# Kernel optimization log

Hardware: AMD Instinct MI355X
Metric: run time of the kernel (lower is better)

Reference implementation:

```python
import jax, jax.numpy as jnp
import numpy as np


def _conv_valid(x, w):
    # x: [B, Cin, H, W], w: [Cout, Cin, K, K], stride 1, no padding
    return jax.lax.conv_general_dilated(
        x, w, window_strides=(1, 1), padding='VALID',
        dimension_numbers=('NCHW', 'OIHW', 'NCHW'))


def _buggy_maxpool(x, k=2):
    # Faithful to the source MaxPool: window of size kxk slides with STRIDE 1,
    # but only the first H//k x W//k positions are kept (top-left region).
    nh = x.shape[2] // k
    nw = x.shape[3] // k
    m = jax.lax.reduce_window(
        x, -jnp.inf, jax.lax.max,
        window_dimensions=(1, 1, k, k),
        window_strides=(1, 1, 1, 1),
        padding='VALID')  # [B, C, H-k+1, W-k+1]
    return m[:, :, :nh, :nw]


def setup_inputs() -> dict:
    key = jax.random.key(0)
    ks = jax.random.split(key, 9)
    B = 8192
    x = jax.random.normal(ks[0], (B, 3, 32, 32), dtype=jnp.float32)
    s = 0.1
    conv1_w = jax.random.normal(ks[1], (6, 3, 5, 5), dtype=jnp.float32) * s
    conv2_w = jax.random.normal(ks[2], (16, 6, 5, 5), dtype=jnp.float32) * s
    fc1_w = jax.random.normal(ks[3], (120, 400), dtype=jnp.float32) * s
    fc1_b = jax.random.normal(ks[4], (120,), dtype=jnp.float32) * s
    fc2_w = jax.random.normal(ks[5], (84, 120), dtype=jnp.float32) * s
    fc2_b = jax.random.normal(ks[6], (84,), dtype=jnp.float32) * s
    fc3_w = jax.random.normal(ks[7], (10, 84), dtype=jnp.float32) * s
    fc3_b = jax.random.normal(ks[8], (10,), dtype=jnp.float32) * s
    return {
        'x': x,
        'conv1_w': conv1_w, 'conv2_w': conv2_w,
        'fc1_w': fc1_w, 'fc1_b': fc1_b,
        'fc2_w': fc2_w, 'fc2_b': fc2_b,
        'fc3_w': fc3_w, 'fc3_b': fc3_b,
    }


def reference(x, conv1_w, conv2_w, fc1_w, fc1_b, fc2_w, fc2_b, fc3_w, fc3_b):
    h = _buggy_maxpool(jax.nn.relu(_conv_valid(x, conv1_w)))   # [B,6,14,14]
    h = _buggy_maxpool(jax.nn.relu(_conv_valid(h, conv2_w)))   # [B,16,5,5]
    h = h.reshape(-1, 16 * 5 * 5)                              # [B,400]
    h = jax.nn.relu(h @ fc1_w.T + fc1_b)                       # [B,120]
    h = jax.nn.relu(h @ fc2_w.T + fc2_b)                       # [B,84]
    return h @ fc3_w.T + fc3_b                                 # [B,10]
```

## Files before the change

kernel.cpp:

```cpp
#include <hip/hip_runtime.h>


typedef float v2f __attribute__((ext_vector_type(2)));
__device__ __forceinline__ v2f mk2(float a, float b) { v2f t; t.x = a; t.y = b; return t; }
__device__ __forceinline__ v2f shfl2(v2f v, int src) {
    v2f r; r.x = __shfl(v.x, src, 64); r.y = __shfl(v.y, src, 64); return r;
}

constexpr int THREADS = 256;
constexpr int IPB = 8;

constexpr int W1P_OFF = 0;
constexpr int W2P_OFF = 452;
constexpr int IMG_BASE = 2852;
constexpr int XS_OFF = 0;
constexpr int P1_OFF = 0;
constexpr int P2_OFF = 0;
constexpr int F1_OFF = 0;
constexpr int F2_OFF = 128;
constexpr int IMG_STRIDE = 720;
constexpr int LDS_FLOATS = IMG_BASE + IPB * IMG_STRIDE;

__device__ __forceinline__ void wave_sync() {
    asm volatile("s_waitcnt lgkmcnt(0)" ::: "memory");
}

extern "C" __global__ __launch_bounds__(THREADS, 4)
void lenet_fused(const float* __restrict__ x,
                 const float* __restrict__ w1,
                 const float* __restrict__ w2,
                 const float* __restrict__ fc1w, const float* __restrict__ fc1b,
                 const float* __restrict__ fc2w, const float* __restrict__ fc2b,
                 const float* __restrict__ fc3w, const float* __restrict__ fc3b,
                 float* __restrict__ out)
{
    __shared__ __align__(16) float lds[LDS_FLOATS];
    const int tid  = threadIdx.x;
    const int lane = tid & 63;
    const int wv   = tid >> 6;
    const int img0 = blockIdx.x * IPB;
    const v2f zero2 = mk2(0.f, 0.f);

    for (int i = tid; i < 450; i += THREADS) {
        int ocp = i / 150, rem = i - ocp * 150, k = rem >> 1, h = rem & 1;
        lds[W1P_OFF + i] = w1[(2 * ocp + h) * 75 + k];
    }
    for (int i = tid; i < 2400; i += THREADS) {
        int ocp = i / 300, rem = i - ocp * 300, k = rem >> 1, h = rem & 1;
        lds[W2P_OFF + i] = w2[(2 * ocp + h) * 150 + k];
    }

    float* baseA = lds + IMG_BASE + (wv * 2) * IMG_STRIDE;
    float* baseB = baseA + IMG_STRIDE;
    {
        const float4* xgA = (const float4*)(x + (size_t)(img0 + wv * 2) * 3072);
        const float4* xgB = (const float4*)(x + (size_t)(img0 + wv * 2 + 1) * 3072);
        float4* dA = (float4*)(baseA + XS_OFF);
        float4* dB = (float4*)(baseB + XS_OFF);
        for (int i = lane; i < 180; i += 64) {
            int c = i / 60, rem = i - c * 60;
            int r = rem >> 2, c4 = rem & 3;
            int src = c * 256 + r * 8 + c4;
            dA[i] = xgA[src];
            dB[i] = xgB[src];
        }
    }
    __syncthreads();

    float* p1A = baseA + P1_OFF;
    float* p1B = baseB + P1_OFF;

    {
        const int l   = (lane < 33) ? lane : 32;
        const int ocp = l / 11;
        const int r   = l - ocp * 11;
        const float4* xsA = (const float4*)(baseA + XS_OFF);
        const float4* xsB = (const float4*)(baseB + XS_OFF);
        const v2f* w1p = (const v2f*)(lds + W1P_OFF);

        v2f accA[11], accB[11];
        #pragma unroll
        for (int c = 0; c < 11; ++c) { accA[c] = zero2; accB[c] = zero2; }

        #pragma unroll
        for (int i = 0; i < 15; ++i) {
            const int ci = i / 5, kr = i - ci * 5;
            const int b = ci * 60 + (r + kr) * 4;
            float4 A0 = xsA[b], A1 = xsA[b + 1], A2 = xsA[b + 2], A3 = xsA[b + 3];
            float4 B0 = xsB[b], B1 = xsB[b + 1], B2 = xsB[b + 2], B3 = xsB[b + 3];
            v2f W[5];
            #pragma unroll
            for (int kc = 0; kc < 5; ++kc) W[kc] = w1p[ocp * 75 + i * 5 + kc];
            float xa[16], xb[16];
            xa[0]=A0.x; xa[1]=A0.y; xa[2]=A0.z;  xa[3]=A0.w;
            xa[4]=A1.x; xa[5]=A1.y; xa[6]=A1.z;  xa[7]=A1.w;
            xa[8]=A2.x; xa[9]=A2.y; xa[10]=A2.z; xa[11]=A2.w;
            xa[12]=A3.x; xa[13]=A3.y; xa[14]=A3.z; xa[15]=A3.w;
            xb[0]=B0.x; xb[1]=B0.y; xb[2]=B0.z;  xb[3]=B0.w;
            xb[4]=B1.x; xb[5]=B1.y; xb[6]=B1.z;  xb[7]=B1.w;
            xb[8]=B2.x; xb[9]=B2.y; xb[10]=B2.z; xb[11]=B2.w;
            xb[12]=B3.x; xb[13]=B3.y; xb[14]=B3.z; xb[15]=B3.w;
            #pragma unroll
            for (int kc = 0; kc < 5; ++kc) {
                #pragma unroll
                for (int c = 0; c < 11; ++c) {
                    accA[c] = __builtin_elementwise_fma(
                        mk2(xa[c + kc], xa[c + kc]), W[kc], accA[c]);
                    accB[c] = __builtin_elementwise_fma(
                        mk2(xb[c + kc], xb[c + kc]), W[kc], accB[c]);
                }
            }
        }

        v2f pmA[10], pmB[10], mA[10], mB[10];
        #pragma unroll
        for (int c = 0; c < 10; ++c) {
            v2f aA0 = __builtin_elementwise_max(accA[c], zero2);
            v2f aA1 = __builtin_elementwise_max(accA[c + 1], zero2);
            pmA[c] = __builtin_elementwise_max(aA0, aA1);
            v2f aB0 = __builtin_elementwise_max(accB[c], zero2);
            v2f aB1 = __builtin_elementwise_max(accB[c + 1], zero2);
            pmB[c] = __builtin_elementwise_max(aB0, aB1);
        }
        #pragma unroll
        for (int c = 0; c < 10; ++c) {
            mA[c] = __builtin_elementwise_max(pmA[c], shfl2(pmA[c], lane + 1));
            mB[c] = __builtin_elementwise_max(pmB[c], shfl2(pmB[c], lane + 1));
        }
        wave_sync();
        if (r < 10) {
            const int oc0 = ocp * 2;
            float2* dA0 = (float2*)(p1A + oc0 * 120 + r * 12);
            float2* dA1 = (float2*)(p1A + (oc0 + 1) * 120 + r * 12);
            float2* dB0 = (float2*)(p1B + oc0 * 120 + r * 12);
            float2* dB1 = (float2*)(p1B + (oc0 + 1) * 120 + r * 12);
            #pragma unroll
            for (int j = 0; j < 5; ++j) {
                dA0[j] = make_float2(mA[2 * j].x, mA[2 * j + 1].x);
                dA1[j] = make_float2(mA[2 * j].y, mA[2 * j + 1].y);
                dB0[j] = make_float2(mB[2 * j].x, mB[2 * j + 1].x);
                dB1[j] = make_float2(mB[2 * j].y, mB[2 * j + 1].y);
            }
        }
    }
    wave_sync();

    float* p2A = baseA + P2_OFF;
    float* p2B = baseB + P2_OFF;
    {
        const int l   = (lane < 48) ? lane : 47;
        const int ocp = l / 6;
        const int r   = l - ocp * 6;
        const float4* pA4 = (const float4*)p1A;
        const float2* pA2 = (const float2*)p1A;
        const float4* pB4 = (const float4*)p1B;
        const float2* pB2 = (const float2*)p1B;
        const v2f* w2p = (const v2f*)(lds + W2P_OFF);

        v2f accA[6], accB[6];
        #pragma unroll
        for (int c = 0; c < 6; ++c) { accA[c] = zero2; accB[c] = zero2; }

        #pragma unroll
        for (int i = 0; i < 30; ++i) {
            const int ci = i / 5, kr = i - ci * 5;
            float4 A0 = pA4[ci * 30 + (r + kr) * 3 + 0];
            float4 A1 = pA4[ci * 30 + (r + kr) * 3 + 1];
            float2 A2 = pA2[ci * 60 + (r + kr) * 6 + 4];
            float4 B0 = pB4[ci * 30 + (r + kr) * 3 + 0];
            float4 B1 = pB4[ci * 30 + (r + kr) * 3 + 1];
            float2 B2 = pB2[ci * 60 + (r + kr) * 6 + 4];
            v2f W[5];
            #pragma unroll
            for (int kc = 0; kc < 5; ++kc) W[kc] = w2p[ocp * 150 + i * 5 + kc];
            float xa[10], xb[10];
            xa[0]=A0.x; xa[1]=A0.y; xa[2]=A0.z; xa[3]=A0.w;
            xa[4]=A1.x; xa[5]=A1.y; xa[6]=A1.z; xa[7]=A1.w;
            xa[8]=A2.x; xa[9]=A2.y;
            xb[0]=B0.x; xb[1]=B0.y; xb[2]=B0.z; xb[3]=B0.w;
            xb[4]=B1.x; xb[5]=B1.y; xb[6]=B1.z; xb[7]=B1.w;
            xb[8]=B2.x; xb[9]=B2.y;
            #pragma unroll
            for (int kc = 0; kc < 5; ++kc) {
                #pragma unroll
                for (int c = 0; c < 6; ++c) {
                    accA[c] = __builtin_elementwise_fma(
                        mk2(xa[c + kc], xa[c + kc]), W[kc], accA[c]);
                    accB[c] = __builtin_elementwise_fma(
                        mk2(xb[c + kc], xb[c + kc]), W[kc], accB[c]);
                }
            }
        }

        v2f pmA[5], pmB[5], mA[5], mB[5];
        #pragma unroll
        for (int c = 0; c < 5; ++c) {
            v2f aA0 = __builtin_elementwise_max(accA[c], zero2);
            v2f aA1 = __builtin_elementwise_max(accA[c + 1], zero2);
            pmA[c] = __builtin_elementwise_max(aA0, aA1);
            v2f aB0 = __builtin_elementwise_max(accB[c], zero2);
            v2f aB1 = __builtin_elementwise_max(accB[c + 1], zero2);
            pmB[c] = __builtin_elementwise_max(aB0, aB1);
        }
        #pragma unroll
        for (int c = 0; c < 5; ++c) {
            mA[c] = __builtin_elementwise_max(pmA[c], shfl2(pmA[c], lane + 1));
            mB[c] = __builtin_elementwise_max(pmB[c], shfl2(pmB[c], lane + 1));
        }
        wave_sync();
        if (r < 5) {
            const int oc0 = ocp * 2;
            #pragma unroll
            for (int c = 0; c < 5; ++c) {
                p2A[oc0 * 25 + r * 5 + c]       = mA[c].x;
                p2A[(oc0 + 1) * 25 + r * 5 + c] = mA[c].y;
                p2B[oc0 * 25 + r * 5 + c]       = mB[c].x;
                p2B[(oc0 + 1) * 25 + r * 5 + c] = mB[c].y;
            }
        }
    }
    __syncthreads();

    float* scr = lds;
    if (tid < 240) {
        const int row  = tid >> 1;
        const int half = tid & 1;
        const float4* wrow = (const float4*)(fc1w + row * 400) + half * 50;
        v2f acc[8];
        #pragma unroll
        for (int im = 0; im < 8; ++im) acc[im] = zero2;
        #pragma unroll 2
        for (int k = 0; k < 50; ++k) {
            float4 w4 = wrow[k];
            const v2f wxy = mk2(w4.x, w4.y), wzw = mk2(w4.z, w4.w);
            #pragma unroll
            for (int im = 0; im < 8; ++im) {
                const float4* ap = (const float4*)(lds + IMG_BASE + im * IMG_STRIDE + P2_OFF) + half * 50;
                float4 a = ap[k];
                acc[im] = __builtin_elementwise_fma(mk2(a.x, a.y), wxy, acc[im]);
                acc[im] = __builtin_elementwise_fma(mk2(a.z, a.w), wzw, acc[im]);
            }
        }
        #pragma unroll
        for (int im = 0; im < 8; ++im)
            scr[im * 240 + row * 2 + half] = acc[im].x + acc[im].y;
    }
    __syncthreads();

    if (tid < 120) {
        const float b = fc1b[tid];
        #pragma unroll
        for (int im = 0; im < 8; ++im) {
            float v = scr[im * 240 + tid * 2] + scr[im * 240 + tid * 2 + 1] + b;
            lds[IMG_BASE + im * IMG_STRIDE + F1_OFF + tid] = fmaxf(v, 0.f);
        }
    }
    __syncthreads();

    if (tid < 84) {
        const int row = tid;
        const float4* wrow = (const float4*)(fc2w + row * 120);
        const float bz = fc2b[row];
        v2f acc[8];
        #pragma unroll
        for (int im = 0; im < 8; ++im) acc[im] = zero2;
        #pragma unroll 2
        for (int k = 0; k < 30; ++k) {
            float4 w4 = wrow[k];
            const v2f wxy = mk2(w4.x, w4.y), wzw = mk2(w4.z, w4.w);
            #pragma unroll
            for (int im = 0; im < 8; ++im) {
                const float4* fp = (const float4*)(lds + IMG_BASE + im * IMG_STRIDE + F1_OFF);
                float4 a = fp[k];
                acc[im] = __builtin_elementwise_fma(mk2(a.x, a.y), wxy, acc[im]);
                acc[im] = __builtin_elementwise_fma(mk2(a.z, a.w), wzw, acc[im]);
            }
        }
        #pragma unroll
        for (int im = 0; im < 8; ++im)
            lds[IMG_BASE + im * IMG_STRIDE + F2_OFF + row] =
                fmaxf(acc[im].x + acc[im].y + bz, 0.f);
    }
    __syncthreads();

    if (tid < 80) {
        const int im  = tid / 10;
        const int row = tid - im * 10;
        const float4* wrow = (const float4*)(fc3w + row * 84);
        const float4* f2 = (const float4*)(lds + IMG_BASE + im * IMG_STRIDE + F2_OFF);
        v2f acc = zero2;
        #pragma unroll
        for (int k = 0; k < 21; ++k) {
            float4 w4 = wrow[k];
            float4 a = f2[k];
            acc = __builtin_elementwise_fma(mk2(a.x, a.y), mk2(w4.x, w4.y), acc);
            acc = __builtin_elementwise_fma(mk2(a.z, a.w), mk2(w4.z, w4.w), acc);
        }
        out[(size_t)(img0 + im) * 10 + row] = acc.x + acc.y + fc3b[row];
    }
}

extern "C" void kernel_launch(void* const* d_in, const int* in_sizes, int n_in,
                              void* d_out, int out_size, void* d_ws, size_t ws_size,
                              hipStream_t stream) {
    const float* x    = (const float*)d_in[0];
    const float* w1   = (const float*)d_in[1];
    const float* w2   = (const float*)d_in[2];
    const float* fc1w = (const float*)d_in[3];
    const float* fc1b = (const float*)d_in[4];
    const float* fc2w = (const float*)d_in[5];
    const float* fc2b = (const float*)d_in[6];
    const float* fc3w = (const float*)d_in[7];
    const float* fc3b = (const float*)d_in[8];
    float* out = (float*)d_out;

    const int B = in_sizes[0] / 3072;
    const int grid = B / IPB;
    lenet_fused<<<grid, THREADS, 0, stream>>>(x, w1, w2, fc1w, fc1b,
                                              fc2w, fc2b, fc3w, fc3b, out);
}
```

Measured before the change: 214.4 us.

## Use one wave per image with 512 threads and padded input layout

Doubles the block to 512 threads so each of the 8 waves handles one image through both conv stages instead of two. The input tile is stored with a padded row stride (5 float4 per row, 75 per channel) and the per-image LDS stride grows to 900 floats. FC1 and FC2 are split across twice as many threads, each covering 4 images. This lowers per-thread register pressure and raises the number of resident waves, at the cost of a larger LDS footprint per block and more work repeated per wave (weight loads, index math).

```diff
diff --git a/kernel.cpp b/kernel.cpp
--- a/kernel.cpp
+++ b/kernel.cpp
@@ -7,7 +7,7 @@
     v2f r; r.x = __shfl(v.x, src, 64); r.y = __shfl(v.y, src, 64); return r;
 }
 
-constexpr int THREADS = 256;
+constexpr int THREADS = 512;
 constexpr int IPB = 8;
 
 constexpr int W1P_OFF = 0;
@@ -18,14 +18,14 @@
 constexpr int P2_OFF = 0;
 constexpr int F1_OFF = 0;
 constexpr int F2_OFF = 128;
-constexpr int IMG_STRIDE = 720;
+constexpr int IMG_STRIDE = 900;
 constexpr int LDS_FLOATS = IMG_BASE + IPB * IMG_STRIDE;
 
 __device__ __forceinline__ void wave_sync() {
     asm volatile("s_waitcnt lgkmcnt(0)" ::: "memory");
 }
 
-extern "C" __global__ __launch_bounds__(THREADS, 4)
+extern "C" __global__ __launch_bounds__(THREADS, 8)
 void lenet_fused(const float* __restrict__ x,
                  const float* __restrict__ w1,
                  const float* __restrict__ w2,
@@ -50,200 +50,161 @@
         lds[W2P_OFF + i] = w2[(2 * ocp + h) * 150 + k];
     }
 
-    float* baseA = lds + IMG_BASE + (wv * 2) * IMG_STRIDE;
-    float* baseB = baseA + IMG_STRIDE;
+    float* base = lds + IMG_BASE + wv * IMG_STRIDE;
     {
-        const float4* xgA = (const float4*)(x + (size_t)(img0 + wv * 2) * 3072);
-        const float4* xgB = (const float4*)(x + (size_t)(img0 + wv * 2 + 1) * 3072);
-        float4* dA = (float4*)(baseA + XS_OFF);
-        float4* dB = (float4*)(baseB + XS_OFF);
+        const float4* xg = (const float4*)(x + (size_t)(img0 + wv) * 3072);
+        float4* d = (float4*)(base + XS_OFF);
         for (int i = lane; i < 180; i += 64) {
             int c = i / 60, rem = i - c * 60;
             int r = rem >> 2, c4 = rem & 3;
-            int src = c * 256 + r * 8 + c4;
-            dA[i] = xgA[src];
-            dB[i] = xgB[src];
-        }
-    }
-    __syncthreads();
-
-    float* p1A = baseA + P1_OFF;
-    float* p1B = baseB + P1_OFF;
+            d[c * 75 + r * 5 + c4] = xg[c * 256 + r * 8 + c4];
+        }
+    }
+    __syncthreads();
+
+    float* p1 = base + P1_OFF;
 
     {
         const int l   = (lane < 33) ? lane : 32;
         const int ocp = l / 11;
         const int r   = l - ocp * 11;
-        const float4* xsA = (const float4*)(baseA + XS_OFF);
-        const float4* xsB = (const float4*)(baseB + XS_OFF);
+        const float4* xs = (const float4*)(base + XS_OFF);
         const v2f* w1p = (const v2f*)(lds + W1P_OFF);
 
-        v2f accA[11], accB[11];
-        #pragma unroll
-        for (int c = 0; c < 11; ++c) { accA[c] = zero2; accB[c] = zero2; }
+        v2f acc[11];
+        #pragma unroll
+        for (int c = 0; c < 11; ++c) acc[c] = zero2;
 
         #pragma unroll
         for (int i = 0; i < 15; ++i) {
             const int ci = i / 5, kr = i - ci * 5;
-            const int b = ci * 60 + (r + kr) * 4;
-            float4 A0 = xsA[b], A1 = xsA[b + 1], A2 = xsA[b + 2], A3 = xsA[b + 3];
-            float4 B0 = xsB[b], B1 = xsB[b + 1], B2 = xsB[b + 2], B3 = xsB[b + 3];
+            const int b = ci * 75 + (r + kr) * 5;
+            float4 A0 = xs[b], A1 = xs[b + 1], A2 = xs[b + 2], A3 = xs[b + 3];
             v2f W[5];
             #pragma unroll
             for (int kc = 0; kc < 5; ++kc) W[kc] = w1p[ocp * 75 + i * 5 + kc];
-            float xa[16], xb[16];
+            float xa[16];
             xa[0]=A0.x; xa[1]=A0.y; xa[2]=A0.z;  xa[3]=A0.w;
             xa[4]=A1.x; xa[5]=A1.y; xa[6]=A1.z;  xa[7]=A1.w;
             xa[8]=A2.x; xa[9]=A2.y; xa[10]=A2.z; xa[11]=A2.w;
             xa[12]=A3.x; xa[13]=A3.y; xa[14]=A3.z; xa[15]=A3.w;
-            xb[0]=B0.x; xb[1]=B0.y; xb[2]=B0.z;  xb[3]=B0.w;
-            xb[4]=B1.x; xb[5]=B1.y; xb[6]=B1.z;  xb[7]=B1.w;
-            xb[8]=B2.x; xb[9]=B2.y; xb[10]=B2.z; xb[11]=B2.w;
-            xb[12]=B3.x; xb[13]=B3.y; xb[14]=B3.z; xb[15]=B3.w;
             #pragma unroll
             for (int kc = 0; kc < 5; ++kc) {
                 #pragma unroll
                 for (int c = 0; c < 11; ++c) {
-                    accA[c] = __builtin_elementwise_fma(
-                        mk2(xa[c + kc], xa[c + kc]), W[kc], accA[c]);
-                    accB[c] = __builtin_elementwise_fma(
-                        mk2(xb[c + kc], xb[c + kc]), W[kc], accB[c]);
+                    acc[c] = __builtin_elementwise_fma(
+                        mk2(xa[c + kc], xa[c + kc]), W[kc], acc[c]);
                 }
             }
         }
 
-        v2f pmA[10], pmB[10], mA[10], mB[10];
+        v2f pm[10], m[10];
         #pragma unroll
         for (int c = 0; c < 10; ++c) {
-            v2f aA0 = __builtin_elementwise_max(accA[c], zero2);
-            v2f aA1 = __builtin_elementwise_max(accA[c + 1], zero2);
-            pmA[c] = __builtin_elementwise_max(aA0, aA1);
-            v2f aB0 = __builtin_elementwise_max(accB[c], zero2);
-            v2f aB1 = __builtin_elementwise_max(accB[c + 1], zero2);
-            pmB[c] = __builtin_elementwise_max(aB0, aB1);
-        }
-        #pragma unroll
-        for (int c = 0; c < 10; ++c) {
-            mA[c] = __builtin_elementwise_max(pmA[c], shfl2(pmA[c], lane + 1));
-            mB[c] = __builtin_elementwise_max(pmB[c], shfl2(pmB[c], lane + 1));
-        }
+            v2f a0 = __builtin_elementwise_max(acc[c], zero2);
+            v2f a1 = __builtin_elementwise_max(acc[c + 1], zero2);
+            pm[c] = __builtin_elementwise_max(a0, a1);
+        }
+        #pragma unroll
+        for (int c = 0; c < 10; ++c)
+            m[c] = __builtin_elementwise_max(pm[c], shfl2(pm[c], lane + 1));
         wave_sync();
         if (r < 10) {
             const int oc0 = ocp * 2;
-            float2* dA0 = (float2*)(p1A + oc0 * 120 + r * 12);
-            float2* dA1 = (float2*)(p1A + (oc0 + 1) * 120 + r * 12);
-            float2* dB0 = (float2*)(p1B + oc0 * 120 + r * 12);
-            float2* dB1 = (float2*)(p1B + (oc0 + 1) * 120 + r * 12);
+            float2* d0 = (float2*)(p1 + oc0 * 120 + r * 12);
+            float2* d1 = (float2*)(p1 + (oc0 + 1) * 120 + r * 12);
             #pragma unroll
             for (int j = 0; j < 5; ++j) {
-                dA0[j] = make_float2(mA[2 * j].x, mA[2 * j + 1].x);
-                dA1[j] = make_float2(mA[2 * j].y, mA[2 * j + 1].y);
-                dB0[j] = make_float2(mB[2 * j].x, mB[2 * j + 1].x);
-                dB1[j] = make_float2(mB[2 * j].y, mB[2 * j + 1].y);
+                d0[j] = make_float2(m[2 * j].x, m[2 * j + 1].x);
+                d1[j] = make_float2(m[2 * j].y, m[2 * j + 1].y);
             }
         }
     }
     wave_sync();
 
-    float* p2A = baseA + P2_OFF;
-    float* p2B = baseB + P2_OFF;
+    float* p2 = base + P2_OFF;
     {
         const int l   = (lane < 48) ? lane : 47;
         const int ocp = l / 6;
         const int r   = l - ocp * 6;
-        const float4* pA4 = (const float4*)p1A;
-        const float2* pA2 = (const float2*)p1A;
-        const float4* pB4 = (const float4*)p1B;
-        const float2* pB2 = (const float2*)p1B;
+        const float4* pa4 = (const float4*)p1;
+        const float2* pa2 = (const float2*)p1;
         const v2f* w2p = (const v2f*)(lds + W2P_OFF);
 
-        v2f accA[6], accB[6];
-        #pragma unroll
-        for (int c = 0; c < 6; ++c) { accA[c] = zero2; accB[c] = zero2; }
+        v2f acc[6];
+        #pragma unroll
+        for (int c = 0; c < 6; ++c) acc[c] = zero2;
 
         #pragma unroll
         for (int i = 0; i < 30; ++i) {
             const int ci = i / 5, kr = i - ci * 5;
-            float4 A0 = pA4[ci * 30 + (r + kr) * 3 + 0];
-            float4 A1 = pA4[ci * 30 + (r + kr) * 3 + 1];
-            float2 A2 = pA2[ci * 60 + (r + kr) * 6 + 4];
-            float4 B0 = pB4[ci * 30 + (r + kr) * 3 + 0];
-            float4 B1 = pB4[ci * 30 + (r + kr) * 3 + 1];
-            float2 B2 = pB2[ci * 60 + (r + kr) * 6 + 4];
+            float4 A0 = pa4[ci * 30 + (r + kr) * 3 + 0];
+            float4 A1 = pa4[ci * 30 + (r + kr) * 3 + 1];
+            float2 A2 = pa2[ci * 60 + (r + kr) * 6 + 4];
             v2f W[5];
             #pragma unroll
             for (int kc = 0; kc < 5; ++kc) W[kc] = w2p[ocp * 150 + i * 5 + kc];
-            float xa[10], xb[10];
+            float xa[10];
             xa[0]=A0.x; xa[1]=A0.y; xa[2]=A0.z; xa[3]=A0.w;
             xa[4]=A1.x; xa[5]=A1.y; xa[6]=A1.z; xa[7]=A1.w;
             xa[8]=A2.x; xa[9]=A2.y;
-            xb[0]=B0.x; xb[1]=B0.y; xb[2]=B0.z; xb[3]=B0.w;
-            xb[4]=B1.x; xb[5]=B1.y; xb[6]=B1.z; xb[7]=B1.w;
-            xb[8]=B2.x; xb[9]=B2.y;
             #pragma unroll
             for (int kc = 0; kc < 5; ++kc) {
                 #pragma unroll
                 for (int c = 0; c < 6; ++c) {
-                    accA[c] = __builtin_elementwise_fma(
-                        mk2(xa[c + kc], xa[c + kc]), W[kc], accA[c]);
-                    accB[c] = __builtin_elementwise_fma(
-                        mk2(xb[c + kc], xb[c + kc]), W[kc], accB[c]);
+                    acc[c] = __builtin_elementwise_fma(
+                        mk2(xa[c + kc], xa[c + kc]), W[kc], acc[c]);
                 }
             }
         }
 
-        v2f pmA[5], pmB[5], mA[5], mB[5];
+        v2f pm[5], m[5];
         #pragma unroll
         for (int c = 0; c < 5; ++c) {
-            v2f aA0 = __builtin_elementwise_max(accA[c], zero2);
-            v2f aA1 = __builtin_elementwise_max(accA[c + 1], zero2);
-            pmA[c] = __builtin_elementwise_max(aA0, aA1);
-            v2f aB0 = __builtin_elementwise_max(accB[c], zero2);
-            v2f aB1 = __builtin_elementwise_max(accB[c + 1], zero2);
-            pmB[c] = __builtin_elementwise_max(aB0, aB1);
-        }
-        #pragma unroll
-        for (int c = 0; c < 5; ++c) {
-            mA[c] = __builtin_elementwise_max(pmA[c], shfl2(pmA[c], lane + 1));
-            mB[c] = __builtin_elementwise_max(pmB[c], shfl2(pmB[c], lane + 1));
-        }
+            v2f a0 = __builtin_elementwise_max(acc[c], zero2);
+            v2f a1 = __builtin_elementwise_max(acc[c + 1], zero2);
+            pm[c] = __builtin_elementwise_max(a0, a1);
+        }
+        #pragma unroll
+        for (int c = 0; c < 5; ++c)
+            m[c] = __builtin_elementwise_max(pm[c], shfl2(pm[c], lane + 1));
         wave_sync();
         if (r < 5) {
             const int oc0 = ocp * 2;
             #pragma unroll
             for (int c = 0; c < 5; ++c) {
-                p2A[oc0 * 25 + r * 5 + c]       = mA[c].x;
-                p2A[(oc0 + 1) * 25 + r * 5 + c] = mA[c].y;
-                p2B[oc0 * 25 + r * 5 + c]       = mB[c].x;
-                p2B[(oc0 + 1) * 25 + r * 5 + c] = mB[c].y;
+                p2[oc0 * 25 + r * 5 + c]       = m[c].x;
+                p2[(oc0 + 1) * 25 + r * 5 + c] = m[c].y;
             }
         }
     }
     __syncthreads();
 
     float* scr = lds;
-    if (tid < 240) {
-        const int row  = tid >> 1;
-        const int half = tid & 1;
+    if (tid < 480) {
+        const int row  = tid >> 2;
+        const int rh   = tid & 3;
+        const int half = rh >> 1;
+        const int imh  = rh & 1;
         const float4* wrow = (const float4*)(fc1w + row * 400) + half * 50;
-        v2f acc[8];
-        #pragma unroll
-        for (int im = 0; im < 8; ++im) acc[im] = zero2;
+        v2f acc[4];
+        #pragma unroll
+        for (int q = 0; q < 4; ++q) acc[q] = zero2;
         #pragma unroll 2
         for (int k = 0; k < 50; ++k) {
             float4 w4 = wrow[k];
             const v2f wxy = mk2(w4.x, w4.y), wzw = mk2(w4.z, w4.w);
             #pragma unroll
-            for (int im = 0; im < 8; ++im) {
-                const float4* ap = (const float4*)(lds + IMG_BASE + im * IMG_STRIDE + P2_OFF) + half * 50;
+            for (int q = 0; q < 4; ++q) {
+                const float4* ap = (const float4*)(lds + IMG_BASE + (imh * 4 + q) * IMG_STRIDE + P2_OFF) + half * 50;
                 float4 a = ap[k];
-                acc[im] = __builtin_elementwise_fma(mk2(a.x, a.y), wxy, acc[im]);
-                acc[im] = __builtin_elementwise_fma(mk2(a.z, a.w), wzw, acc[im]);
-            }
-        }
-        #pragma unroll
-        for (int im = 0; im < 8; ++im)
-            scr[im * 240 + row * 2 + half] = acc[im].x + acc[im].y;
+                acc[q] = __builtin_elementwise_fma(mk2(a.x, a.y), wxy, acc[q]);
+                acc[q] = __builtin_elementwise_fma(mk2(a.z, a.w), wzw, acc[q]);
+            }
+        }
+        #pragma unroll
+        for (int q = 0; q < 4; ++q)
+            scr[(imh * 4 + q) * 240 + row * 2 + half] = acc[q].x + acc[q].y;
     }
     __syncthreads();
 
@@ -257,29 +218,30 @@
     }
     __syncthreads();
 
-    if (tid < 84) {
-        const int row = tid;
+    if (tid < 168) {
+        const int row = tid >> 1;
+        const int imh = tid & 1;
         const float4* wrow = (const float4*)(fc2w + row * 120);
         const float bz = fc2b[row];
-        v2f acc[8];
-        #pragma unroll
-        for (int im = 0; im < 8; ++im) acc[im] = zero2;
+        v2f acc[4];
+        #pragma unroll
+        for (int q = 0; q < 4; ++q) acc[q] = zero2;
         #pragma unroll 2
         for (int k = 0; k < 30; ++k) {
             float4 w4 = wrow[k];
             const v2f wxy = mk2(w4.x, w4.y), wzw = mk2(w4.z, w4.w);
             #pragma unroll
-            for (int im = 0; im < 8; ++im) {
-                const float4* fp = (const float4*)(lds + IMG_BASE + im * IMG_STRIDE + F1_OFF);
+            for (int q = 0; q < 4; ++q) {
+                const float4* fp = (const float4*)(lds + IMG_BASE + (imh * 4 + q) * IMG_STRIDE + F1_OFF);
                 float4 a = fp[k];
-                acc[im] = __builtin_elementwise_fma(mk2(a.x, a.y), wxy, acc[im]);
-                acc[im] = __builtin_elementwise_fma(mk2(a.z, a.w), wzw, acc[im]);
-            }
-        }
-        #pragma unroll
-        for (int im = 0; im < 8; ++im)
-            lds[IMG_BASE + im * IMG_STRIDE + F2_OFF + row] =
-                fmaxf(acc[im].x + acc[im].y + bz, 0.f);
+                acc[q] = __builtin_elementwise_fma(mk2(a.x, a.y), wxy, acc[q]);
+                acc[q] = __builtin_elementwise_fma(mk2(a.z, a.w), wzw, acc[q]);
+            }
+        }
+        #pragma unroll
+        for (int q = 0; q < 4; ++q)
+            lds[IMG_BASE + (imh * 4 + q) * IMG_STRIDE + F2_OFF + row] =
+                fmaxf(acc[q].x + acc[q].y + bz, 0.f);
     }
     __syncthreads();
 
```

Result: faster. 208.8 us (-2.6%).

## Double block size to 16 images and pad LDS image rows

Applied to the files above, without the earlier changes.

Doubles the block to 512 threads and 16 images, so each of the 8 waves still handles 2 images while the per-block LDS weight staging and the FC weight reads from global are shared across twice as many images. The input tile rows in LDS are padded from 4 to 5 float4 per row (stride 900), presumably to reduce LDS bank conflicts in the conv1 reads. The FC layers are re-split so more threads work on them, each over 4-image groups in two passes, and the fc1 partial-sum scratch moves into per-image LDS space. The cost is a larger LDS footprint per block, which may limit occupancy, and a launch-bounds hint of 8 that may force register caps.

```diff
diff --git a/kernel.cpp b/kernel.cpp
--- a/kernel.cpp
+++ b/kernel.cpp
@@ -7,8 +7,8 @@
     v2f r; r.x = __shfl(v.x, src, 64); r.y = __shfl(v.y, src, 64); return r;
 }
 
-constexpr int THREADS = 256;
-constexpr int IPB = 8;
+constexpr int THREADS = 512;
+constexpr int IPB = 16;
 
 constexpr int W1P_OFF = 0;
 constexpr int W2P_OFF = 452;
@@ -16,16 +16,17 @@
 constexpr int XS_OFF = 0;
 constexpr int P1_OFF = 0;
 constexpr int P2_OFF = 0;
+constexpr int SCR_OFF = 400;
 constexpr int F1_OFF = 0;
 constexpr int F2_OFF = 128;
-constexpr int IMG_STRIDE = 720;
+constexpr int IMG_STRIDE = 900;
 constexpr int LDS_FLOATS = IMG_BASE + IPB * IMG_STRIDE;
 
 __device__ __forceinline__ void wave_sync() {
     asm volatile("s_waitcnt lgkmcnt(0)" ::: "memory");
 }
 
-extern "C" __global__ __launch_bounds__(THREADS, 4)
+extern "C" __global__ __launch_bounds__(THREADS, 8)
 void lenet_fused(const float* __restrict__ x,
                  const float* __restrict__ w1,
                  const float* __restrict__ w2,
@@ -60,9 +61,10 @@
         for (int i = lane; i < 180; i += 64) {
             int c = i / 60, rem = i - c * 60;
             int r = rem >> 2, c4 = rem & 3;
+            int dst = c * 75 + r * 5 + c4;
             int src = c * 256 + r * 8 + c4;
-            dA[i] = xgA[src];
-            dB[i] = xgB[src];
+            dA[dst] = xgA[src];
+            dB[dst] = xgB[src];
         }
     }
     __syncthreads();
@@ -85,7 +87,7 @@
         #pragma unroll
         for (int i = 0; i < 15; ++i) {
             const int ci = i / 5, kr = i - ci * 5;
-            const int b = ci * 60 + (r + kr) * 4;
+            const int b = ci * 75 + (r + kr) * 5;
             float4 A0 = xsA[b], A1 = xsA[b + 1], A2 = xsA[b + 2], A3 = xsA[b + 3];
             float4 B0 = xsB[b], B1 = xsB[b + 1], B2 = xsB[b + 2], B3 = xsB[b + 3];
             v2f W[5];
@@ -221,69 +223,81 @@
     }
     __syncthreads();
 
-    float* scr = lds;
-    if (tid < 240) {
-        const int row  = tid >> 1;
-        const int half = tid & 1;
+    if (tid < 480) {
+        const int row  = tid >> 2;
+        const int rh   = tid & 3;
+        const int half = rh >> 1;
+        const int imh  = rh & 1;
         const float4* wrow = (const float4*)(fc1w + row * 400) + half * 50;
-        v2f acc[8];
-        #pragma unroll
-        for (int im = 0; im < 8; ++im) acc[im] = zero2;
-        #pragma unroll 2
-        for (int k = 0; k < 50; ++k) {
-            float4 w4 = wrow[k];
-            const v2f wxy = mk2(w4.x, w4.y), wzw = mk2(w4.z, w4.w);
-            #pragma unroll
-            for (int im = 0; im < 8; ++im) {
-                const float4* ap = (const float4*)(lds + IMG_BASE + im * IMG_STRIDE + P2_OFF) + half * 50;
-                float4 a = ap[k];
-                acc[im] = __builtin_elementwise_fma(mk2(a.x, a.y), wxy, acc[im]);
-                acc[im] = __builtin_elementwise_fma(mk2(a.z, a.w), wzw, acc[im]);
-            }
-        }
-        #pragma unroll
-        for (int im = 0; im < 8; ++im)
-            scr[im * 240 + row * 2 + half] = acc[im].x + acc[im].y;
+        #pragma unroll
+        for (int pass = 0; pass < 2; ++pass) {
+            const int ib = pass * 8 + imh * 4;
+            v2f acc[4];
+            #pragma unroll
+            for (int q = 0; q < 4; ++q) acc[q] = zero2;
+            #pragma unroll 2
+            for (int k = 0; k < 50; ++k) {
+                float4 w4 = wrow[k];
+                const v2f wxy = mk2(w4.x, w4.y), wzw = mk2(w4.z, w4.w);
+                #pragma unroll
+                for (int q = 0; q < 4; ++q) {
+                    const float4* ap = (const float4*)(lds + IMG_BASE + (ib + q) * IMG_STRIDE + P2_OFF) + half * 50;
+                    float4 a = ap[k];
+                    acc[q] = __builtin_elementwise_fma(mk2(a.x, a.y), wxy, acc[q]);
+                    acc[q] = __builtin_elementwise_fma(mk2(a.z, a.w), wzw, acc[q]);
+                }
+            }
+            #pragma unroll
+            for (int q = 0; q < 4; ++q)
+                lds[IMG_BASE + (ib + q) * IMG_STRIDE + SCR_OFF + row * 2 + half] =
+                    acc[q].x + acc[q].y;
+        }
     }
     __syncthreads();
 
     if (tid < 120) {
         const float b = fc1b[tid];
         #pragma unroll
-        for (int im = 0; im < 8; ++im) {
-            float v = scr[im * 240 + tid * 2] + scr[im * 240 + tid * 2 + 1] + b;
+        for (int im = 0; im < 16; ++im) {
+            const float* s = lds + IMG_BASE + im * IMG_STRIDE + SCR_OFF;
+            float v = s[tid * 2] + s[tid * 2 + 1] + b;
             lds[IMG_BASE + im * IMG_STRIDE + F1_OFF + tid] = fmaxf(v, 0.f);
         }
     }
     __syncthreads();
 
-    if (tid < 84) {
-        const int row = tid;
+    if (tid < 168) {
+        const int row = tid >> 1;
+        const int imh = tid & 1;
         const float4* wrow = (const float4*)(fc2w + row * 120);
         const float bz = fc2b[row];
-        v2f acc[8];
-        #pragma unroll
-        for (int im = 0; im < 8; ++im) acc[im] = zero2;
-        #pragma unroll 2
-        for (int k = 0; k < 30; ++k) {
-            float4 w4 = wrow[k];
-            const v2f wxy = mk2(w4.x, w4.y), wzw = mk2(w4.z, w4.w);
-            #pragma unroll
-            for (int im = 0; im < 8; ++im) {
-                const float4* fp = (const float4*)(lds + IMG_BASE + im * IMG_STRIDE + F1_OFF);
-                float4 a = fp[k];
-                acc[im] = __builtin_elementwise_fma(mk2(a.x, a.y), wxy, acc[im]);
-                acc[im] = __builtin_elementwise_fma(mk2(a.z, a.w), wzw, acc[im]);
-            }
-        }
-        #pragma unroll
-        for (int im = 0; im < 8; ++im)
-            lds[IMG_BASE + im * IMG_STRIDE + F2_OFF + row] =
-                fmaxf(acc[im].x + acc[im].y + bz, 0.f);
-    }
-    __syncthreads();
-
-    if (tid < 80) {
+        #pragma unroll
+        for (int pass = 0; pass < 2; ++pass) {
+            const int ib = pass * 8 + imh * 4;
+            v2f acc[4];
+            #pragma unroll
+            for (int q = 0; q < 4; ++q) acc[q] = zero2;
+            #pragma unroll 2
+            for (int k = 0; k < 30; ++k) {
+                float4 w4 = wrow[k];
+                const v2f wxy = mk2(w4.x, w4.y), wzw = mk2(w4.z, w4.w);
+                #pragma unroll
+                for (int q = 0; q < 4; ++q) {
+                    const float4* fp = (const float4*)(lds + IMG_BASE + (ib + q) * IMG_STRIDE + F1_OFF);
+                    float4 a = fp[k];
+                    acc[q] = __builtin_elementwise_fma(mk2(a.x, a.y), wxy, acc[q]);
+                    acc[q] = __builtin_elementwise_fma(mk2(a.z, a.w), wzw, acc[q]);
+                }
+            }
+            #pragma unroll
+            for (int q = 0; q < 4; ++q)
+                lds[IMG_BASE + (ib + q) * IMG_STRIDE + F2_OFF + row] =
+                    fmaxf(acc[q].x + acc[q].y + bz, 0.f);
+        }
+    }
+    __syncthreads();
+
+    if (tid < 160) {
         const int im  = tid / 10;
         const int row = tid - im * 10;
         const float4* wrow = (const float4*)(fc3w + row * 84);
```

Result: faster. 209.9 us (-2.1%).
